# Kernel optimization log

Hardware: AMD Instinct MI355X
Metric: run time of the kernel (lower is better)

## Reference

```python
import jax, jax.numpy as jnp
import numpy as np
import math

HEADS = 32
DIM_HEAD = 64
DM = HEADS * DIM_HEAD  # 2048
B, S = 2, 1024
BITS = 3
N_LEVELS = 2 ** BITS
N_GROUPS = (DIM_HEAD + 2) // 3  # 22
PAD = (3 - DIM_HEAD % 3) % 3    # 2
EPS_NORM = 1e-8
EPS_RMS = 1e-6


def _rotors_to_matrices(r):
    # r: (G,4) unit rotors [s, b12, b13, b23] -> (G,3,3) rotation matrices
    s, p, q, rr = r[:, 0], r[:, 1], r[:, 2], r[:, 3]
    s2, p2, q2, r2 = s * s, p * p, q * q, rr * rr
    M = np.zeros((r.shape[0], 3, 3), dtype=np.float32)
    M[:, 0, 0] = s2 - p2 - q2 + r2
    M[:, 0, 1] = 2 * s * p - 2 * q * rr
    M[:, 0, 2] = 2 * s * q + 2 * p * rr
    M[:, 1, 0] = -2 * s * p - 2 * q * rr
    M[:, 1, 1] = s2 - p2 + q2 - r2
    M[:, 1, 2] = 2 * s * rr - 2 * p * q
    M[:, 2, 0] = -2 * s * q + 2 * p * rr
    M[:, 2, 1] = -2 * s * rr - 2 * p * q
    M[:, 2, 2] = s2 + p2 - q2 - r2
    return M


def _make_compressor(seed):
    rng = np.random.default_rng(seed)
    rot = rng.standard_normal((N_GROUPS, 4)).astype(np.float32)
    rot /= np.linalg.norm(rot, axis=-1, keepdims=True)
    M = _rotors_to_matrices(rot)
    sigma = 1.0 / math.sqrt(DIM_HEAD)  # Lloyd-Max for N(0, 1/d)
    C = np.linspace(-3 * sigma, 3 * sigma, N_LEVELS, dtype=np.float32)
    return jnp.asarray(M), jnp.asarray(np.ascontiguousarray(M.transpose(0, 2, 1))), jnp.asarray(C)


def setup_inputs() -> dict:
    key = jax.random.key(0)
    ks = jax.random.split(key, 8)
    x = jax.random.normal(ks[0], (B, S, DM), dtype=jnp.float32)
    w_scale = 0.02
    Wq = jax.random.normal(ks[1], (DM, DM), dtype=jnp.float32) * w_scale
    Wk = jax.random.normal(ks[2], (DM, DM), dtype=jnp.float32) * w_scale
    Wv = jax.random.normal(ks[3], (DM, DM), dtype=jnp.float32) * w_scale
    Wo = jax.random.normal(ks[4], (DM, DM), dtype=jnp.float32) * w_scale
    qn_w = jnp.ones((DM,), dtype=jnp.float32)
    kn_w = jnp.ones((DM,), dtype=jnp.float32)
    Mk, Mtk, Ck = _make_compressor(42)
    Mv, Mtv, Cv = _make_compressor(4200)
    return {"x": x, "Wq": Wq, "Wk": Wk, "Wv": Wv, "Wo": Wo,
            "qn_w": qn_w, "kn_w": kn_w,
            "Mk": Mk, "Mtk": Mtk, "Ck": Ck,
            "Mv": Mv, "Mtv": Mtv, "Cv": Cv}


def _rmsnorm(x, w):
    return x * jax.lax.rsqrt(jnp.mean(x * x, axis=-1, keepdims=True) + EPS_RMS) * w


def _quant_roundtrip(h, M, Mt, C):
    """RotorQuant compress+decompress. h: (B,H,S,Dh) -> (B,H,S,Dh)."""
    norms = jnp.maximum(jnp.linalg.norm(h, axis=-1, keepdims=True), EPS_NORM)
    xu = h / norms
    xu = jnp.pad(xu, ((0, 0), (0, 0), (0, 0), (0, PAD)))
    g = xu.reshape(h.shape[0], h.shape[1], h.shape[2], N_GROUPS, 3)
    rot = jnp.einsum('bhsgi,gij->bhsgj', g, M)
    flat = rot.reshape(h.shape[0], h.shape[1], h.shape[2], N_GROUPS * 3)
    # nearest-centroid quantization (uint8 indices in original)
    idx = jnp.argmin(jnp.abs(flat[..., None] - C), axis=-1)
    deq = C[idx]
    g2 = deq.reshape(h.shape[0], h.shape[1], h.shape[2], N_GROUPS, 3)
    der = jnp.einsum('bhsgi,gij->bhsgj', g2, Mt)
    out = der.reshape(h.shape[0], h.shape[1], h.shape[2], N_GROUPS * 3)[..., :DIM_HEAD]
    return out * norms


def reference(x, Wq, Wk, Wv, Wo, qn_w, kn_w, Mk, Mtk, Ck, Mv, Mtv, Cv):
    b, s, _ = x.shape
    v = x @ Wv
    q = _rmsnorm(x @ Wq, qn_w)
    k = _rmsnorm(x @ Wk, kn_w)
    # split heads -> (B,H,S,Dh)
    qh = q.reshape(b, s, HEADS, DIM_HEAD).transpose(0, 2, 1, 3)
    kh = k.reshape(b, s, HEADS, DIM_HEAD).transpose(0, 2, 1, 3)
    vh = v.reshape(b, s, HEADS, DIM_HEAD).transpose(0, 2, 1, 3)
    # per-head rotor quantization roundtrip of K and V
    kh = _quant_roundtrip(kh, Mk, Mtk, Ck)
    vh = _quant_roundtrip(vh, Mv, Mtv, Cv)
    # scaled dot-product attention
    scores = jnp.einsum('bhqd,bhkd->bhqk', qh, kh) / math.sqrt(DIM_HEAD)
    probs = jax.nn.softmax(scores, axis=-1)
    o = jnp.einsum('bhqk,bhkd->bhqd', probs, vh)
    o = o.transpose(0, 2, 1, 3).reshape(b, s, DM)
    return o @ Wo
```

## Files before the change

kernel.cpp:

```cpp
#include <hip/hip_runtime.h>
#include <hip/hip_bf16.h>
#include <math.h>

#define HEADS 32
#define DIM_HEAD 64
#define DM 2048
#define BATCH 2
#define SEQ 1024
#define NROWS (BATCH * SEQ)
#define NVEC (NROWS * HEADS)
#define N_GROUPS 22
#define N_LEVELS 8
#define EPS_NORM 1e-8f
#define EPS_RMS 1e-6f

typedef float f32x4 __attribute__((ext_vector_type(4)));
typedef __bf16 bf16x8 __attribute__((ext_vector_type(8)));
typedef unsigned short u16x8 __attribute__((ext_vector_type(8)));
typedef unsigned short u16x4 __attribute__((ext_vector_type(4)));

__device__ __forceinline__ unsigned short f2bf(float x) {
  union { float f; unsigned u; } v; v.f = x;
  unsigned r = v.u + 0x7fffu + ((v.u >> 16) & 1u);
  return (unsigned short)(r >> 16);
}
__device__ __forceinline__ float bf2f(unsigned short h) {
  union { unsigned u; float f; } v; v.u = ((unsigned)h) << 16;
  return v.f;
}
__device__ __forceinline__ bf16x8 ldfrag(const unsigned short* p) {
  return __builtin_bit_cast(bf16x8, *(const u16x8*)p);
}
#define MFMA16(a, b, c) __builtin_amdgcn_mfma_f32_16x16x32_bf16((a), (b), (c), 0, 0, 0)

__device__ __forceinline__ void stage16(const unsigned short* g, unsigned short* lds) {
  __builtin_amdgcn_global_load_lds(
      (const __attribute__((address_space(1))) unsigned int*)g,
      (__attribute__((address_space(3))) unsigned int*)lds, 16, 0, 0);
}

__global__ __launch_bounds__(256) void split_convert_kernel(
    const float* __restrict__ X, unsigned short* __restrict__ hi,
    unsigned short* __restrict__ lo, int n8) {
  const int i = blockIdx.x * 256 + threadIdx.x;
  if (i >= n8) return;
  const float4 a = ((const float4*)X)[2 * i];
  const float4 b = ((const float4*)X)[2 * i + 1];
  const float v[8] = {a.x, a.y, a.z, a.w, b.x, b.y, b.z, b.w};
  u16x8 h, l;
#pragma unroll
  for (int j = 0; j < 8; ++j) {
    const unsigned short hh = f2bf(v[j]);
    h[j] = hh;
    l[j] = f2bf(v[j] - bf2f(hh));
  }
  ((u16x8*)hi)[i] = h;
  if (lo) ((u16x8*)lo)[i] = l;
}

__global__ __launch_bounds__(256) void transpose_split_batch_kernel(
    const float* __restrict__ W0, const float* __restrict__ W1,
    const float* __restrict__ W2, const float* __restrict__ W3,
    unsigned short* __restrict__ T0h, unsigned short* __restrict__ T1h,
    unsigned short* __restrict__ T1l, unsigned short* __restrict__ T2h,
    unsigned short* __restrict__ T2l, unsigned short* __restrict__ T3h) {
  const int z = blockIdx.z;
  const float* W = (z == 0) ? W0 : (z == 1) ? W1 : (z == 2) ? W2 : W3;
  unsigned short* Th = (z == 0) ? T0h : (z == 1) ? T1h : (z == 2) ? T2h : T3h;
  unsigned short* Tl = (z == 1) ? T1l : (z == 2) ? T2l : nullptr;

  __shared__ float S[64][65];
  const int t = threadIdx.x;
  const int tk = blockIdx.y * 64, tm = blockIdx.x * 64;
  {
    const int r = t >> 2, cs = (t & 3) * 16;
    const float* src = W + (size_t)(tk + r) * DM + tm + cs;
#pragma unroll
    for (int j = 0; j < 16; j += 4) {
      float4 v = *(const float4*)(src + j);
      S[r][cs + j] = v.x; S[r][cs + j + 1] = v.y;
      S[r][cs + j + 2] = v.z; S[r][cs + j + 3] = v.w;
    }
  }
  __syncthreads();
  const int m = t >> 2, ks = (t & 3) * 16;
  u16x8 h0, h1, l0, l1;
#pragma unroll
  for (int j = 0; j < 8; ++j) {
    const float v = S[ks + j][m];
    const unsigned short hh = f2bf(v);
    h0[j] = hh; l0[j] = f2bf(v - bf2f(hh));
  }
#pragma unroll
  for (int j = 0; j < 8; ++j) {
    const float v = S[ks + 8 + j][m];
    const unsigned short hh = f2bf(v);
    h1[j] = hh; l1[j] = f2bf(v - bf2f(hh));
  }
  const size_t o = (size_t)(tm + m) * DM + tk + ks;
  *(u16x8*)&Th[o] = h0; *(u16x8*)&Th[o + 8] = h1;
  if (Tl) { *(u16x8*)&Tl[o] = l0; *(u16x8*)&Tl[o + 8] = l1; }
}

__global__ __launch_bounds__(256) void qkv_gemm_kernel(
    const unsigned short* __restrict__ Ahi, const unsigned short* __restrict__ Alo,
    const unsigned short* __restrict__ Bhi, const unsigned short* __restrict__ Blo,
    float* __restrict__ q, float* __restrict__ k, float* __restrict__ v) {
  __shared__ unsigned short lAhi[128 * 32];
  __shared__ unsigned short lBhi[128 * 32];
  __shared__ unsigned short lAlo[128 * 32];
  __shared__ unsigned short lBlo[128 * 32];

  const int t = threadIdx.x;
  const int lane = t & 63, wave = t >> 6;
  const int wr = wave >> 1, wc = wave & 1;
  const int gm0 = blockIdx.y * 128;
  const int gnc = blockIdx.x * 128;
  const int seg = gnc >> 11;
  const bool split = (seg != 0);
  const int lrsub = lane >> 2;
  const int lcsub = lane & 3;

  f32x4 acc[4][4] = {};

  for (int kt = 0; kt < DM; kt += 32) {
    __syncthreads();
#pragma unroll
    for (int rg = wave; rg < 8; rg += 4) {
      const int lrow = rg * 16 + lrsub;
      const int c = lcsub ^ ((lrow >> 1) & 3);
      const size_t goffA = (size_t)(gm0 + lrow) * DM + kt + c * 8;
      const size_t goffB = (size_t)(gnc + lrow) * DM + kt + c * 8;
      stage16(Ahi + goffA, lAhi + rg * 512);
      stage16(Bhi + goffB, lBhi + rg * 512);
      if (split) {
        stage16(Alo + goffA, lAlo + rg * 512);
        stage16(Blo + goffB, lBlo + rg * 512);
      }
    }
    __syncthreads();

    bf16x8 ah[4], bh[4], al[4], bl[4];
#pragma unroll
    for (int i = 0; i < 4; ++i) {
      const int mrow = wr * 64 + i * 16 + (lane & 15);
      const int offa = mrow * 32 + (((lane >> 4) ^ ((mrow >> 1) & 3)) << 3);
      ah[i] = ldfrag(&lAhi[offa]);
      const int nrow = wc * 64 + i * 16 + (lane & 15);
      const int offb = nrow * 32 + (((lane >> 4) ^ ((nrow >> 1) & 3)) << 3);
      bh[i] = ldfrag(&lBhi[offb]);
      if (split) {
        al[i] = ldfrag(&lAlo[offa]);
        bl[i] = ldfrag(&lBlo[offb]);
      }
    }
#pragma unroll
    for (int i = 0; i < 4; ++i)
#pragma unroll
      for (int j = 0; j < 4; ++j) {
        acc[i][j] = MFMA16(ah[i], bh[j], acc[i][j]);
        if (split) {
          acc[i][j] = MFMA16(ah[i], bl[j], acc[i][j]);
          acc[i][j] = MFMA16(al[i], bh[j], acc[i][j]);
        }
      }
  }

  float* C = (seg == 0) ? q : (seg == 1) ? k : v;
  const int gn0 = gnc & 2047;
#pragma unroll
  for (int i = 0; i < 4; ++i) {
    const int row = gm0 + wr * 64 + i * 16 + ((lane >> 4) << 2);
#pragma unroll
    for (int j = 0; j < 4; ++j) {
      const int col = gn0 + wc * 64 + j * 16 + (lane & 15);
#pragma unroll
      for (int r = 0; r < 4; ++r)
        C[(size_t)(row + r) * DM + col] = acc[i][j][r];
    }
  }
}

__global__ __launch_bounds__(256) void gemm_out_splitk_kernel(
    const unsigned short* __restrict__ Ahi, const unsigned short* __restrict__ Bt,
    float* __restrict__ Cpart) {
  __shared__ unsigned short lAhi[128 * 32];
  __shared__ unsigned short lBhi[128 * 32];

  const int t = threadIdx.x;
  const int lane = t & 63, wave = t >> 6;
  const int wr = wave >> 1, wc = wave & 1;
  const int gm0 = blockIdx.y * 128, gn0 = blockIdx.x * 128;
  const int z = blockIdx.z;
  const int k0 = z * (DM / 2);
  const int lrsub = lane >> 2;
  const int lcsub = lane & 3;

  f32x4 acc[4][4] = {};

  for (int kt = k0; kt < k0 + DM / 2; kt += 32) {
    __syncthreads();
#pragma unroll
    for (int rg = wave; rg < 8; rg += 4) {
      const int lrow = rg * 16 + lrsub;
      const int c = lcsub ^ ((lrow >> 1) & 3);
      stage16(Ahi + (size_t)(gm0 + lrow) * DM + kt + c * 8, lAhi + rg * 512);
      stage16(Bt + (size_t)(gn0 + lrow) * DM + kt + c * 8, lBhi + rg * 512);
    }
    __syncthreads();

    bf16x8 ah[4], bh[4];
#pragma unroll
    for (int i = 0; i < 4; ++i) {
      const int mrow = wr * 64 + i * 16 + (lane & 15);
      ah[i] = ldfrag(&lAhi[mrow * 32 + (((lane >> 4) ^ ((mrow >> 1) & 3)) << 3)]);
      const int nrow = wc * 64 + i * 16 + (lane & 15);
      bh[i] = ldfrag(&lBhi[nrow * 32 + (((lane >> 4) ^ ((nrow >> 1) & 3)) << 3)]);
    }
#pragma unroll
    for (int i = 0; i < 4; ++i)
#pragma unroll
      for (int j = 0; j < 4; ++j)
        acc[i][j] = MFMA16(ah[i], bh[j], acc[i][j]);
  }

  float* C = Cpart + (size_t)z * NROWS * DM;
#pragma unroll
  for (int i = 0; i < 4; ++i) {
    const int row = gm0 + wr * 64 + i * 16 + ((lane >> 4) << 2);
#pragma unroll
    for (int j = 0; j < 4; ++j) {
      const int col = gn0 + wc * 64 + j * 16 + (lane & 15);
#pragma unroll
      for (int r = 0; r < 4; ++r)
        C[(size_t)(row + r) * DM + col] = acc[i][j][r];
    }
  }
}

__global__ __launch_bounds__(256) void add2_f4_kernel(
    const float* __restrict__ a, const float* __restrict__ b,
    float* __restrict__ o, int n4) {
  const int i = blockIdx.x * 256 + threadIdx.x;
  if (i >= n4) return;
  const float4 x = ((const float4*)a)[i];
  const float4 y = ((const float4*)b)[i];
  ((float4*)o)[i] = make_float4(x.x + y.x, x.y + y.y, x.z + y.z, x.w + y.w);
}

__device__ __forceinline__ float wave_sum(float x) {
#pragma unroll
  for (int o = 32; o > 0; o >>= 1) x += __shfl_xor(x, o, 64);
  return x;
}

__global__ __launch_bounds__(256) void rmsnorm_kernel(
    float* __restrict__ y, const float* __restrict__ w) {
  __shared__ float rbuf[4];
  const int row = blockIdx.x;
  float* p = y + (size_t)row * DM;
  const int t = threadIdx.x;
  const int wave = t >> 6, lane = t & 63;

  float ss = 0.f;
#pragma unroll
  for (int c = t; c < DM; c += 256) { float v = p[c]; ss += v * v; }
  ss = wave_sum(ss);
  if (lane == 0) rbuf[wave] = ss;
  __syncthreads();
  ss = rbuf[0] + rbuf[1] + rbuf[2] + rbuf[3];
  const float scale = rsqrtf(ss * (1.0f / DM) + EPS_RMS);
#pragma unroll
  for (int c = t; c < DM; c += 256) p[c] = p[c] * scale * w[c];
}

__global__ __launch_bounds__(256) void rmsnorm_split_kernel(
    const float* __restrict__ y, const float* __restrict__ w,
    unsigned short* __restrict__ hi, unsigned short* __restrict__ lo,
    float post) {
  __shared__ float rbuf[4];
  const int row = blockIdx.x;
  const float* p = y + (size_t)row * DM;
  const int t = threadIdx.x;
  const int wave = t >> 6, lane = t & 63;

  const int c0 = t * 8;
  float4 a = *(const float4*)(p + c0);
  float4 b = *(const float4*)(p + c0 + 4);
  float v[8] = {a.x, a.y, a.z, a.w, b.x, b.y, b.z, b.w};
  float ss = 0.f;
#pragma unroll
  for (int j = 0; j < 8; ++j) ss += v[j] * v[j];
  ss = wave_sum(ss);
  if (lane == 0) rbuf[wave] = ss;
  __syncthreads();
  ss = rbuf[0] + rbuf[1] + rbuf[2] + rbuf[3];
  const float scale = rsqrtf(ss * (1.0f / DM) + EPS_RMS) * post;

  u16x8 hv, lv;
#pragma unroll
  for (int j = 0; j < 8; ++j) {
    const float val = v[j] * scale * w[c0 + j];
    const unsigned short hh = f2bf(val);
    hv[j] = hh; lv[j] = f2bf(val - bf2f(hh));
  }
  *(u16x8*)&hi[(size_t)row * DM + c0] = hv;
  *(u16x8*)&lo[(size_t)row * DM + c0] = lv;
}

__device__ __forceinline__ float qnearest(float v, const float* __restrict__ C) {
  float best = C[0];
  float bd = fabsf(v - C[0]);
#pragma unroll
  for (int i = 1; i < N_LEVELS; ++i) {
    float d = fabsf(v - C[i]);
    if (d < bd) { bd = d; best = C[i]; }
  }
  return best;
}

template <bool WRITE_BF>
__global__ __launch_bounds__(256) void quant_kernel(
    float* __restrict__ kv, const float* __restrict__ M,
    const float* __restrict__ Mt, const float* __restrict__ C,
    unsigned short* __restrict__ hi, unsigned short* __restrict__ lo) {
  const int vec = blockIdx.x * blockDim.x + threadIdx.x;
  if (vec >= NVEC) return;
  float* p = kv + (size_t)vec * DIM_HEAD;

  float h[66];
  float ss = 0.f;
#pragma unroll
  for (int d = 0; d < DIM_HEAD; ++d) { h[d] = p[d]; ss += h[d] * h[d]; }
  float norm = fmaxf(sqrtf(ss), EPS_NORM);
  const float inv = 1.0f / norm;
#pragma unroll
  for (int d = 0; d < DIM_HEAD; ++d) h[d] *= inv;
  h[64] = 0.f; h[65] = 0.f;

#pragma unroll
  for (int g = 0; g < N_GROUPS; ++g) {
    const float* Mg  = M  + g * 9;
    const float* Mtg = Mt + g * 9;
    const float a0 = h[3 * g + 0], a1 = h[3 * g + 1], a2 = h[3 * g + 2];
    const float r0 = a0 * Mg[0] + a1 * Mg[3] + a2 * Mg[6];
    const float r1 = a0 * Mg[1] + a1 * Mg[4] + a2 * Mg[7];
    const float r2 = a0 * Mg[2] + a1 * Mg[5] + a2 * Mg[8];
    const float d0 = qnearest(r0, C);
    const float d1 = qnearest(r1, C);
    const float d2 = qnearest(r2, C);
    h[3 * g + 0] = d0 * Mtg[0] + d1 * Mtg[3] + d2 * Mtg[6];
    h[3 * g + 1] = d0 * Mtg[1] + d1 * Mtg[4] + d2 * Mtg[7];
    h[3 * g + 2] = d0 * Mtg[2] + d1 * Mtg[5] + d2 * Mtg[8];
  }
  if (WRITE_BF) {
#pragma unroll
    for (int g8 = 0; g8 < 8; ++g8) {
      u16x8 hv, lv;
#pragma unroll
      for (int j = 0; j < 8; ++j) {
        const float val = h[g8 * 8 + j] * norm;
        const unsigned short hh = f2bf(val);
        hv[j] = hh; lv[j] = f2bf(val - bf2f(hh));
      }
      *(u16x8*)&hi[(size_t)vec * DIM_HEAD + g8 * 8] = hv;
      *(u16x8*)&lo[(size_t)vec * DIM_HEAD + g8 * 8] = lv;
    }
  } else {
#pragma unroll
    for (int d = 0; d < DIM_HEAD; ++d) p[d] = h[d] * norm;
  }
}

__global__ __launch_bounds__(256) void vt_split_kernel(
    const float* __restrict__ v, unsigned short* __restrict__ hi,
    unsigned short* __restrict__ lo) {
  __shared__ float T[64][65];
  const int s0 = blockIdx.x * 64;
  const int bh = blockIdx.y;
  const int b = bh >> 5, h = bh & 31;
  const int t = threadIdx.x;
  {
    const int sr = t >> 2, dseg = (t & 3) * 16;
    const float* src = v + ((size_t)(b * SEQ + s0 + sr) * DM + h * 64 + dseg);
#pragma unroll
    for (int j = 0; j < 16; j += 4) {
      float4 a = *(const float4*)(src + j);
      T[sr][dseg + j] = a.x; T[sr][dseg + j + 1] = a.y;
      T[sr][dseg + j + 2] = a.z; T[sr][dseg + j + 3] = a.w;
    }
  }
  __syncthreads();
  const int d = t >> 2, sseg = (t & 3) * 16;
  u16x8 h0, h1, l0, l1;
#pragma unroll
  for (int j = 0; j < 8; ++j) {
    const float val = T[sseg + j][d];
    const unsigned short hh = f2bf(val);
    h0[j] = hh; l0[j] = f2bf(val - bf2f(hh));
  }
#pragma unroll
  for (int j = 0; j < 8; ++j) {
    const float val = T[sseg + 8 + j][d];
    const unsigned short hh = f2bf(val);
    h1[j] = hh; l1[j] = f2bf(val - bf2f(hh));
  }
  const size_t o = (size_t)(bh * 64 + d) * SEQ + s0 + sseg;
  *(u16x8*)&hi[o] = h0; *(u16x8*)&hi[o + 8] = h1;
  *(u16x8*)&lo[o] = l0; *(u16x8*)&lo[o + 8] = l1;
}

__global__ __launch_bounds__(256) void attn_mfma_kernel(
    const unsigned short* __restrict__ qhi, const unsigned short* __restrict__ qlo,
    const unsigned short* __restrict__ khi, const unsigned short* __restrict__ klo,
    const unsigned short* __restrict__ vthi, const unsigned short* __restrict__ vtlo,
    unsigned short* __restrict__ ohi) {
  __shared__ unsigned short Ks_h[4096], Ks_l[4096];
  __shared__ unsigned short Vt_h[4096], Vt_l[4096];
  __shared__ unsigned short Ps_h[4096], Ps_l[4096];
  __shared__ float alpha_s[4][16];
  __shared__ float l_s[4][16];

  const int qt = blockIdx.x;
  const int bh = blockIdx.y;
  const int h = bh & 31, b = bh >> 5;
  const int q0 = qt * 64;
  const int t = threadIdx.x, lane = t & 63, w = t >> 6;
  const int quad = lane >> 4, l15 = lane & 15;
  const int srow = lane >> 3, schunk = lane & 7;

  auto stage = [&](const unsigned short* g, int stride, unsigned short* arr) {
#pragma unroll
    for (int it = 0; it < 2; ++it) {
      const int r = w * 16 + it * 8 + srow;
      const int c = schunk ^ (r & 7);
      stage16(g + (size_t)r * stride + c * 8, arr + (w * 16 + it * 8) * 64);
    }
  };

  stage(qhi + ((size_t)(b * SEQ + q0) * DM + h * 64), DM, Ps_h);
  stage(qlo + ((size_t)(b * SEQ + q0) * DM + h * 64), DM, Ps_l);
  __syncthreads();
  bf16x8 qh[2], ql[2];
#pragma unroll
  for (int ks = 0; ks < 2; ++ks) {
    const int row = w * 16 + l15;
    const int off = row * 64 + (((quad + 4 * ks) ^ (row & 7)) << 3);
    qh[ks] = ldfrag(&Ps_h[off]);
    ql[ks] = ldfrag(&Ps_l[off]);
  }

  f32x4 acc[4] = {};
  float m_prev[4] = {-INFINITY, -INFINITY, -INFINITY, -INFINITY};
  float lsum[4] = {0.f, 0.f, 0.f, 0.f};

  const unsigned short* gkh = khi + ((size_t)(b * SEQ) * DM + h * 64);
  const unsigned short* gkl = klo + ((size_t)(b * SEQ) * DM + h * 64);
  const unsigned short* gvh = vthi + (size_t)(bh * 64) * SEQ;
  const unsigned short* gvl = vtlo + (size_t)(bh * 64) * SEQ;

  for (int kt = 0; kt < SEQ; kt += 64) {
    __syncthreads();
    stage(gkh + (size_t)kt * DM, DM, Ks_h);
    stage(gkl + (size_t)kt * DM, DM, Ks_l);
    stage(gvh + kt, SEQ, Vt_h);
    stage(gvl + kt, SEQ, Vt_l);
    __syncthreads();

    f32x4 s[4] = {};
#pragma unroll
    for (int nt = 0; nt < 4; ++nt) {
#pragma unroll
      for (int ks = 0; ks < 2; ++ks) {
        const int row = nt * 16 + l15;
        const int off = row * 64 + (((quad + 4 * ks) ^ (row & 7)) << 3);
        const bf16x8 kh = ldfrag(&Ks_h[off]);
        const bf16x8 kl = ldfrag(&Ks_l[off]);
        s[nt] = MFMA16(qh[ks], kh, s[nt]);
        s[nt] = MFMA16(qh[ks], kl, s[nt]);
        s[nt] = MFMA16(ql[ks], kh, s[nt]);
      }
    }

    float asave[4];
#pragma unroll
    for (int r = 0; r < 4; ++r) {
      float mx = fmaxf(fmaxf(s[0][r], s[1][r]), fmaxf(s[2][r], s[3][r]));
#pragma unroll
      for (int off = 1; off < 16; off <<= 1) mx = fmaxf(mx, __shfl_xor(mx, off, 64));
      const float mn = fmaxf(m_prev[r], mx);
      const float al = __expf(m_prev[r] - mn);
      float rs = 0.f;
#pragma unroll
      for (int nt = 0; nt < 4; ++nt) {
        const float e = __expf(s[nt][r] - mn);
        s[nt][r] = e; rs += e;
      }
#pragma unroll
      for (int off = 1; off < 16; off <<= 1) rs += __shfl_xor(rs, off, 64);
      lsum[r] = lsum[r] * al + rs;
      m_prev[r] = mn;
      asave[r] = al;
      const int prow = w * 16 + quad * 4 + r;
#pragma unroll
      for (int nt = 0; nt < 4; ++nt) {
        const int kk = nt * 16 + l15;
        const int off2 = prow * 64 + (((kk >> 3) ^ (prow & 7)) << 3) + (kk & 7);
        const unsigned short hh = f2bf(s[nt][r]);
        Ps_h[off2] = hh;
        Ps_l[off2] = f2bf(s[nt][r] - bf2f(hh));
      }
    }

    if (l15 == 0) {
#pragma unroll
      for (int r = 0; r < 4; ++r) alpha_s[w][quad * 4 + r] = asave[r];
    }
    const float alph = alpha_s[w][l15];
#pragma unroll
    for (int mt = 0; mt < 4; ++mt) acc[mt] *= alph;

#pragma unroll
    for (int mt = 0; mt < 4; ++mt) {
#pragma unroll
      for (int ks = 0; ks < 2; ++ks) {
        const int drow = mt * 16 + l15;
        const int offv = drow * 64 + (((quad + 4 * ks) ^ (drow & 7)) << 3);
        const bf16x8 vh = ldfrag(&Vt_h[offv]);
        const bf16x8 vl = ldfrag(&Vt_l[offv]);
        const int prow = w * 16 + l15;
        const int offp = prow * 64 + (((quad + 4 * ks) ^ (prow & 7)) << 3);
        const bf16x8 ph = ldfrag(&Ps_h[offp]);
        const bf16x8 pl = ldfrag(&Ps_l[offp]);
        acc[mt] = MFMA16(vh, ph, acc[mt]);
        acc[mt] = MFMA16(vh, pl, acc[mt]);
        acc[mt] = MFMA16(vl, ph, acc[mt]);
      }
    }
  }

  if (l15 == 0) {
#pragma unroll
    for (int r = 0; r < 4; ++r) l_s[w][quad * 4 + r] = lsum[r];
  }
  const float inv = 1.0f / l_s[w][l15];
  const size_t obase = (size_t)(b * SEQ + q0 + w * 16 + l15) * DM + h * 64;
#pragma unroll
  for (int mt = 0; mt < 4; ++mt) {
    u16x4 ov;
#pragma unroll
    for (int r = 0; r < 4; ++r) ov[r] = f2bf(acc[mt][r] * inv);
    *(u16x4*)&ohi[obase + mt * 16 + quad * 4] = ov;
  }
}

extern "C" void kernel_launch(void* const* d_in, const int* in_sizes, int n_in,
                              void* d_out, int out_size, void* d_ws, size_t ws_size,
                              hipStream_t stream) {
  const float* x    = (const float*)d_in[0];
  const float* Wq   = (const float*)d_in[1];
  const float* Wk   = (const float*)d_in[2];
  const float* Wv   = (const float*)d_in[3];
  const float* Wo   = (const float*)d_in[4];
  const float* qn_w = (const float*)d_in[5];
  const float* kn_w = (const float*)d_in[6];
  const float* Mk   = (const float*)d_in[7];
  const float* Mtk  = (const float*)d_in[8];
  const float* Ck   = (const float*)d_in[9];
  const float* Mv   = (const float*)d_in[10];
  const float* Mtv  = (const float*)d_in[11];
  const float* Cv   = (const float*)d_in[12];
  float* out = (float*)d_out;

  const size_t MBb = 1024ull * 1024ull;
  const size_t SEG = (size_t)DM * DM;
  char* w = (char*)d_ws;
  float* qb = (float*)(w + 0 * MBb);
  float* kb = (float*)(w + 16 * MBb);
  float* vb = (float*)(w + 32 * MBb);
  unsigned short* xhi     = (unsigned short*)(w + 48 * MBb);
  unsigned short* xlo     = (unsigned short*)(w + 56 * MBb);
  unsigned short* wcat_hi = (unsigned short*)(w + 64 * MBb);
  unsigned short* wcat_lo = (unsigned short*)(w + 88 * MBb);
  unsigned short* wot     = (unsigned short*)(w + 112 * MBb);
  unsigned short* q_hi  = wcat_hi;
  unsigned short* k_hi  = wcat_hi + SEG;
  unsigned short* k_lo  = wcat_hi + 2 * SEG;
  unsigned short* q_lo  = wcat_lo;
  unsigned short* vt_hi = wcat_lo + SEG;
  unsigned short* vt_lo = wcat_lo + 2 * SEG;
  unsigned short* o_hi  = xhi;
  float* opart = (float*)(w + 0 * MBb);

  const int n8 = (NROWS * DM) / 8;

  split_convert_kernel<<<n8 / 256, 256, 0, stream>>>(x, xhi, xlo, n8);
  transpose_split_batch_kernel<<<dim3(DM / 64, DM / 64, 4), 256, 0, stream>>>(
      Wq, Wk, Wv, Wo,
      wcat_hi, wcat_hi + SEG, wcat_lo + SEG, wcat_hi + 2 * SEG, wcat_lo + 2 * SEG, wot);

  qkv_gemm_kernel<<<dim3(3 * DM / 128, NROWS / 128), 256, 0, stream>>>(
      xhi, xlo, wcat_hi, wcat_lo, qb, kb, vb);

  rmsnorm_kernel<<<NROWS, 256, 0, stream>>>(kb, kn_w);
  rmsnorm_split_kernel<<<NROWS, 256, 0, stream>>>(qb, qn_w, q_hi, q_lo, 0.125f);

  quant_kernel<true ><<<NVEC / 256, 256, 0, stream>>>(kb, Mk, Mtk, Ck, k_hi, k_lo);
  quant_kernel<false><<<NVEC / 256, 256, 0, stream>>>(vb, Mv, Mtv, Cv, nullptr, nullptr);
  vt_split_kernel<<<dim3(SEQ / 64, BATCH * HEADS), 256, 0, stream>>>(vb, vt_hi, vt_lo);

  attn_mfma_kernel<<<dim3(SEQ / 64, BATCH * HEADS), 256, 0, stream>>>(
      q_hi, q_lo, k_hi, k_lo, vt_hi, vt_lo, o_hi);

  gemm_out_splitk_kernel<<<dim3(DM / 128, NROWS / 128, 2), 256, 0, stream>>>(
      o_hi, wot, opart);
  add2_f4_kernel<<<(NROWS * DM / 4 + 255) / 256, 256, 0, stream>>>(
      opart, opart + (size_t)NROWS * DM, out, NROWS * DM / 4);
}
```

Measured before the change: 482.3 us.

## Process 128 queries per attention block so K/V tiles are reused twice

After: 507.8 us. 1.05x slower.

```diff
diff --git a/kernel.cpp b/kernel.cpp
--- a/kernel.cpp
+++ b/kernel.cpp
@@ -417,42 +417,43 @@
     unsigned short* __restrict__ ohi) {
   __shared__ unsigned short Ks_h[4096], Ks_l[4096];
   __shared__ unsigned short Vt_h[4096], Vt_l[4096];
-  __shared__ unsigned short Ps_h[4096], Ps_l[4096];
-  __shared__ float alpha_s[4][16];
-  __shared__ float l_s[4][16];
+  __shared__ unsigned short Ps_h[8192], Ps_l[8192];
 
   const int qt = blockIdx.x;
   const int bh = blockIdx.y;
   const int h = bh & 31, b = bh >> 5;
-  const int q0 = qt * 64;
+  const int q0 = qt * 128;
   const int t = threadIdx.x, lane = t & 63, w = t >> 6;
   const int quad = lane >> 4, l15 = lane & 15;
   const int srow = lane >> 3, schunk = lane & 7;
 
-  auto stage = [&](const unsigned short* g, int stride, unsigned short* arr) {
-#pragma unroll
-    for (int it = 0; it < 2; ++it) {
-      const int r = w * 16 + it * 8 + srow;
+  auto stage = [&](const unsigned short* g, int stride, unsigned short* arr,
+                   int rowbase, int its) {
+    for (int it = 0; it < its; ++it) {
+      const int r = rowbase + it * 8 + srow;
       const int c = schunk ^ (r & 7);
-      stage16(g + (size_t)r * stride + c * 8, arr + (w * 16 + it * 8) * 64);
+      stage16(g + (size_t)r * stride + c * 8, arr + (rowbase + it * 8) * 64);
     }
   };
 
-  stage(qhi + ((size_t)(b * SEQ + q0) * DM + h * 64), DM, Ps_h);
-  stage(qlo + ((size_t)(b * SEQ + q0) * DM + h * 64), DM, Ps_l);
+  stage(qhi + ((size_t)(b * SEQ + q0) * DM + h * 64), DM, Ps_h, w * 32, 4);
+  stage(qlo + ((size_t)(b * SEQ + q0) * DM + h * 64), DM, Ps_l, w * 32, 4);
   __syncthreads();
-  bf16x8 qh[2], ql[2];
-#pragma unroll
-  for (int ks = 0; ks < 2; ++ks) {
-    const int row = w * 16 + l15;
-    const int off = row * 64 + (((quad + 4 * ks) ^ (row & 7)) << 3);
-    qh[ks] = ldfrag(&Ps_h[off]);
-    ql[ks] = ldfrag(&Ps_l[off]);
-  }
-
-  f32x4 acc[4] = {};
-  float m_prev[4] = {-INFINITY, -INFINITY, -INFINITY, -INFINITY};
-  float lsum[4] = {0.f, 0.f, 0.f, 0.f};
+  bf16x8 qh[2][2], ql[2][2];
+#pragma unroll
+  for (int qs = 0; qs < 2; ++qs)
+#pragma unroll
+    for (int ks = 0; ks < 2; ++ks) {
+      const int row = w * 32 + qs * 16 + l15;
+      const int off = row * 64 + (((quad + 4 * ks) ^ (row & 7)) << 3);
+      qh[qs][ks] = ldfrag(&Ps_h[off]);
+      ql[qs][ks] = ldfrag(&Ps_l[off]);
+    }
+
+  f32x4 acc[2][4] = {};
+  float m_prev[2][4] = {{-INFINITY, -INFINITY, -INFINITY, -INFINITY},
+                        {-INFINITY, -INFINITY, -INFINITY, -INFINITY}};
+  float lsum[2][4] = {{0.f, 0.f, 0.f, 0.f}, {0.f, 0.f, 0.f, 0.f}};
 
   const unsigned short* gkh = khi + ((size_t)(b * SEQ) * DM + h * 64);
   const unsigned short* gkl = klo + ((size_t)(b * SEQ) * DM + h * 64);
@@ -461,65 +462,89 @@
 
   for (int kt = 0; kt < SEQ; kt += 64) {
     __syncthreads();
-    stage(gkh + (size_t)kt * DM, DM, Ks_h);
-    stage(gkl + (size_t)kt * DM, DM, Ks_l);
-    stage(gvh + kt, SEQ, Vt_h);
-    stage(gvl + kt, SEQ, Vt_l);
+    stage(gkh + (size_t)kt * DM, DM, Ks_h, w * 16, 2);
+    stage(gkl + (size_t)kt * DM, DM, Ks_l, w * 16, 2);
+    stage(gvh + kt, SEQ, Vt_h, w * 16, 2);
+    stage(gvl + kt, SEQ, Vt_l, w * 16, 2);
     __syncthreads();
 
-    f32x4 s[4] = {};
+    f32x4 s[2][4] = {};
 #pragma unroll
     for (int nt = 0; nt < 4; ++nt) {
+      bf16x8 kh[2], kl[2];
 #pragma unroll
       for (int ks = 0; ks < 2; ++ks) {
         const int row = nt * 16 + l15;
         const int off = row * 64 + (((quad + 4 * ks) ^ (row & 7)) << 3);
-        const bf16x8 kh = ldfrag(&Ks_h[off]);
-        const bf16x8 kl = ldfrag(&Ks_l[off]);
-        s[nt] = MFMA16(qh[ks], kh, s[nt]);
-        s[nt] = MFMA16(qh[ks], kl, s[nt]);
-        s[nt] = MFMA16(ql[ks], kh, s[nt]);
-      }
-    }
-
-    float asave[4];
-#pragma unroll
-    for (int r = 0; r < 4; ++r) {
-      float mx = fmaxf(fmaxf(s[0][r], s[1][r]), fmaxf(s[2][r], s[3][r]));
-#pragma unroll
-      for (int off = 1; off < 16; off <<= 1) mx = fmaxf(mx, __shfl_xor(mx, off, 64));
-      const float mn = fmaxf(m_prev[r], mx);
-      const float al = __expf(m_prev[r] - mn);
-      float rs = 0.f;
-#pragma unroll
-      for (int nt = 0; nt < 4; ++nt) {
-        const float e = __expf(s[nt][r] - mn);
-        s[nt][r] = e; rs += e;
-      }
-#pragma unroll
-      for (int off = 1; off < 16; off <<= 1) rs += __shfl_xor(rs, off, 64);
-      lsum[r] = lsum[r] * al + rs;
-      m_prev[r] = mn;
-      asave[r] = al;
-      const int prow = w * 16 + quad * 4 + r;
-#pragma unroll
-      for (int nt = 0; nt < 4; ++nt) {
-        const int kk = nt * 16 + l15;
-        const int off2 = prow * 64 + (((kk >> 3) ^ (prow & 7)) << 3) + (kk & 7);
-        const unsigned short hh = f2bf(s[nt][r]);
-        Ps_h[off2] = hh;
-        Ps_l[off2] = f2bf(s[nt][r] - bf2f(hh));
-      }
-    }
-
-    if (l15 == 0) {
-#pragma unroll
-      for (int r = 0; r < 4; ++r) alpha_s[w][quad * 4 + r] = asave[r];
-    }
-    const float alph = alpha_s[w][l15];
-#pragma unroll
-    for (int mt = 0; mt < 4; ++mt) acc[mt] *= alph;
-
+        kh[ks] = ldfrag(&Ks_h[off]);
+        kl[ks] = ldfrag(&Ks_l[off]);
+      }
+#pragma unroll
+      for (int qs = 0; qs < 2; ++qs)
+#pragma unroll
+        for (int ks = 0; ks < 2; ++ks) {
+          s[qs][nt] = MFMA16(qh[qs][ks], kh[ks], s[qs][nt]);
+          s[qs][nt] = MFMA16(qh[qs][ks], kl[ks], s[qs][nt]);
+          s[qs][nt] = MFMA16(ql[qs][ks], kh[ks], s[qs][nt]);
+        }
+    }
+
+    float alph[2];
+#pragma unroll
+    for (int qs = 0; qs < 2; ++qs) {
+      float asave[4];
+#pragma unroll
+      for (int r = 0; r < 4; ++r) {
+        float mx = fmaxf(fmaxf(s[qs][0][r], s[qs][1][r]),
+                         fmaxf(s[qs][2][r], s[qs][3][r]));
+#pragma unroll
+        for (int off = 1; off < 16; off <<= 1) mx = fmaxf(mx, __shfl_xor(mx, off, 64));
+        const float mn = fmaxf(m_prev[qs][r], mx);
+        const float al = __expf(m_prev[qs][r] - mn);
+        float rs = 0.f;
+#pragma unroll
+        for (int nt = 0; nt < 4; ++nt) {
+          const float e = __expf(s[qs][nt][r] - mn);
+          s[qs][nt][r] = e; rs += e;
+        }
+#pragma unroll
+        for (int off = 1; off < 16; off <<= 1) rs += __shfl_xor(rs, off, 64);
+        lsum[qs][r] = lsum[qs][r] * al + rs;
+        m_prev[qs][r] = mn;
+        asave[r] = al;
+        const int prow = w * 32 + qs * 16 + quad * 4 + r;
+#pragma unroll
+        for (int nt = 0; nt < 4; ++nt) {
+          const int kk = nt * 16 + l15;
+          const int off2 = prow * 64 + (((kk >> 3) ^ (prow & 7)) << 3) + (kk & 7);
+          const unsigned short hh = f2bf(s[qs][nt][r]);
+          Ps_h[off2] = hh;
+          Ps_l[off2] = f2bf(s[qs][nt][r] - bf2f(hh));
+        }
+      }
+      const int src = (l15 >> 2) << 4;
+      const float a0 = __shfl(asave[0], src, 64);
+      const float a1 = __shfl(asave[1], src, 64);
+      const float a2 = __shfl(asave[2], src, 64);
+      const float a3 = __shfl(asave[3], src, 64);
+      const int rr = l15 & 3;
+      alph[qs] = (rr == 0) ? a0 : (rr == 1) ? a1 : (rr == 2) ? a2 : a3;
+    }
+#pragma unroll
+    for (int qs = 0; qs < 2; ++qs)
+#pragma unroll
+      for (int mt = 0; mt < 4; ++mt) acc[qs][mt] *= alph[qs];
+
+    bf16x8 ph[2][2], pl[2][2];
+#pragma unroll
+    for (int qs = 0; qs < 2; ++qs)
+#pragma unroll
+      for (int ks = 0; ks < 2; ++ks) {
+        const int prow = w * 32 + qs * 16 + l15;
+        const int offp = prow * 64 + (((quad + 4 * ks) ^ (prow & 7)) << 3);
+        ph[qs][ks] = ldfrag(&Ps_h[offp]);
+        pl[qs][ks] = ldfrag(&Ps_l[offp]);
+      }
 #pragma unroll
     for (int mt = 0; mt < 4; ++mt) {
 #pragma unroll
@@ -528,29 +553,35 @@
         const int offv = drow * 64 + (((quad + 4 * ks) ^ (drow & 7)) << 3);
         const bf16x8 vh = ldfrag(&Vt_h[offv]);
         const bf16x8 vl = ldfrag(&Vt_l[offv]);
-        const int prow = w * 16 + l15;
-        const int offp = prow * 64 + (((quad + 4 * ks) ^ (prow & 7)) << 3);
-        const bf16x8 ph = ldfrag(&Ps_h[offp]);
-        const bf16x8 pl = ldfrag(&Ps_l[offp]);
-        acc[mt] = MFMA16(vh, ph, acc[mt]);
-        acc[mt] = MFMA16(vh, pl, acc[mt]);
-        acc[mt] = MFMA16(vl, ph, acc[mt]);
-      }
-    }
-  }
-
-  if (l15 == 0) {
-#pragma unroll
-    for (int r = 0; r < 4; ++r) l_s[w][quad * 4 + r] = lsum[r];
-  }
-  const float inv = 1.0f / l_s[w][l15];
-  const size_t obase = (size_t)(b * SEQ + q0 + w * 16 + l15) * DM + h * 64;
-#pragma unroll
-  for (int mt = 0; mt < 4; ++mt) {
-    u16x4 ov;
-#pragma unroll
-    for (int r = 0; r < 4; ++r) ov[r] = f2bf(acc[mt][r] * inv);
-    *(u16x4*)&ohi[obase + mt * 16 + quad * 4] = ov;
+#pragma unroll
+        for (int qs = 0; qs < 2; ++qs) {
+          acc[qs][mt] = MFMA16(vh, ph[qs][ks], acc[qs][mt]);
+          acc[qs][mt] = MFMA16(vh, pl[qs][ks], acc[qs][mt]);
+          acc[qs][mt] = MFMA16(vl, ph[qs][ks], acc[qs][mt]);
+        }
+      }
+    }
+  }
+
+#pragma unroll
+  for (int qs = 0; qs < 2; ++qs) {
+    const int src = (l15 >> 2) << 4;
+    const float a0 = __shfl(lsum[qs][0], src, 64);
+    const float a1 = __shfl(lsum[qs][1], src, 64);
+    const float a2 = __shfl(lsum[qs][2], src, 64);
+    const float a3 = __shfl(lsum[qs][3], src, 64);
+    const int rr = l15 & 3;
+    const float lq = (rr == 0) ? a0 : (rr == 1) ? a1 : (rr == 2) ? a2 : a3;
+    const float inv = 1.0f / lq;
+    const size_t obase =
+        (size_t)(b * SEQ + q0 + w * 32 + qs * 16 + l15) * DM + h * 64;
+#pragma unroll
+    for (int mt = 0; mt < 4; ++mt) {
+      u16x4 ov;
+#pragma unroll
+      for (int r = 0; r < 4; ++r) ov[r] = f2bf(acc[qs][mt][r] * inv);
+      *(u16x4*)&ohi[obase + mt * 16 + quad * 4] = ov;
+    }
   }
 }
 
@@ -609,7 +640,7 @@
   quant_kernel<false><<<NVEC / 256, 256, 0, stream>>>(vb, Mv, Mtv, Cv, nullptr, nullptr);
   vt_split_kernel<<<dim3(SEQ / 64, BATCH * HEADS), 256, 0, stream>>>(vb, vt_hi, vt_lo);
 
-  attn_mfma_kernel<<<dim3(SEQ / 64, BATCH * HEADS), 256, 0, stream>>>(
+  attn_mfma_kernel<<<dim3(SEQ / 128, BATCH * HEADS), 256, 0, stream>>>(
       q_hi, q_lo, k_hi, k_lo, vt_hi, vt_lo, o_hi);
 
   gemm_out_splitk_kernel<<<dim3(DM / 128, NROWS / 128, 2), 256, 0, stream>>>(
```
